# Optimization experiments

Measured on AMD Instinct MI355X. Metric: run time of the kernel, lower is better.

The kernel has to match this reference:

```python
import jax, jax.numpy as jnp
import numpy as np

C = 256      # in_channels
NH = 4       # n_heads
NG = 32      # GroupNorm num_groups
EPS = 1e-5   # torch GroupNorm default eps


def _conv1x1(x, w, b):
    # 1x1 conv == per-pixel channel matmul. x: (B,C,H,W), w: (O,C), b: (O,)
    return jnp.einsum('oc,bchw->bohw', w, x) + b[None, :, None, None]


def _groupnorm(x, gamma, beta):
    b, c, h, w = x.shape
    xg = x.reshape(b, NG, c // NG, h, w)
    mu = xg.mean(axis=(2, 3, 4), keepdims=True)
    var = xg.var(axis=(2, 3, 4), keepdims=True)
    xn = ((xg - mu) * jax.lax.rsqrt(var + EPS)).reshape(b, c, h, w)
    return xn * gamma[None, :, None, None] + beta[None, :, None, None]


def setup_inputs() -> dict:
    key = jax.random.key(0)
    ks = jax.random.split(key, 5)
    B, H, W = 2, 64, 64
    s = 1.0 / np.sqrt(C).astype(np.float32)
    return {
        'x': jax.random.normal(ks[0], (B, C, H, W), jnp.float32),
        'gamma': jnp.ones((C,), jnp.float32),
        'beta': jnp.zeros((C,), jnp.float32),
        'wq': jax.random.normal(ks[1], (C, C), jnp.float32) * s,
        'bq': jnp.zeros((C,), jnp.float32),
        'wk': jax.random.normal(ks[2], (C, C), jnp.float32) * s,
        'bk': jnp.zeros((C,), jnp.float32),
        'wv': jax.random.normal(ks[3], (C, C), jnp.float32) * s,
        'bv': jnp.zeros((C,), jnp.float32),
        'wp': jax.random.normal(ks[4], (C, C), jnp.float32) * s,
        'bp': jnp.zeros((C,), jnp.float32),
    }


def reference(x, gamma, beta, wq, bq, wk, bk, wv, bv, wp, bp):
    b, c, h, w = x.shape
    c_ = c // NH  # head dim
    hn = _groupnorm(x, gamma, beta)
    # NOTE: original splits channels as (head_dim, n_heads) with head_dim leading
    q = _conv1x1(hn, wq, bq).reshape(b, c_, NH, h * w)
    k = _conv1x1(hn, wk, bk).reshape(b, c_, NH, h * w)
    v = _conv1x1(hn, wv, bv).reshape(b, c_, NH, h * w)
    scores = jnp.einsum('bcnq,bcnk->bqkn', q, k) * (c_ ** -0.5)  # (B,S,S,NH)
    attn = jax.nn.softmax(scores, axis=2)  # softmax over key axis
    out = jnp.einsum('bcnd,bqdn->bcnq', v, attn).reshape(b, c, h, w)
    return x + _conv1x1(out, wp, bp)
```

## Files before the change

kernel.cpp:

```cpp
#include <hip/hip_runtime.h>

#define CH 256
#define NHEAD 4
#define HD 64
#define SP 4096
#define NB 2
#define QSCALE 0.1803368801111204f

typedef __attribute__((ext_vector_type(8))) short bf16x8;
typedef __attribute__((ext_vector_type(4))) float f32x4;
typedef unsigned int u32;
typedef unsigned short u16;

__device__ inline u16 b16(float f) {
    u32 u = __float_as_uint(f);
    return (u16)((u + 0x8000u) >> 16);
}
__device__ inline float fexp2(float x) { return __builtin_amdgcn_exp2f(x); }

__global__ __launch_bounds__(256) void prep_kernel(
    const float* __restrict__ x, float2* __restrict__ part,
    const float* __restrict__ wq, const float* __restrict__ wk,
    const float* __restrict__ wv, const float* __restrict__ wp,
    u16* __restrict__ wqb, u16* __restrict__ wkb,
    u16* __restrict__ wvb, u16* __restrict__ wpb)
{
    int tid = threadIdx.x;
    if (blockIdx.x < 256) {
        int bgq = blockIdx.x;
        int bg = bgq >> 2, qtr = bgq & 3;
        const float4* xp = (const float4*)(x + (size_t)bg * 8 * SP) + qtr * 2048;
        float s = 0.f, ss = 0.f;
        for (int i = tid; i < 2048; i += 256) {
            float4 u = xp[i];
            s  += (u.x + u.y) + (u.z + u.w);
            ss += (u.x * u.x + u.y * u.y) + (u.z * u.z + u.w * u.w);
        }
#pragma unroll
        for (int off = 32; off > 0; off >>= 1) {
            s  += __shfl_down(s, off);
            ss += __shfl_down(ss, off);
        }
        __shared__ float ws_s[4], ws_q[4];
        int w = tid >> 6;
        if ((tid & 63) == 0) { ws_s[w] = s; ws_q[w] = ss; }
        __syncthreads();
        if (tid == 0)
            part[bgq] = make_float2(ws_s[0] + ws_s[1] + ws_s[2] + ws_s[3],
                                    ws_q[0] + ws_q[1] + ws_q[2] + ws_q[3]);
    } else {
        int idx = (blockIdx.x - 256) * 256 + tid;
        int m = idx >> 16, i = idx & 65535;
        if (m == 0)      wqb[i] = b16(wq[i] * QSCALE);
        else if (m == 1) wkb[i] = b16(wk[i]);
        else if (m == 2) wvb[i] = b16(wv[i]);
        else {
            int c = i >> 8, chan = i & 255;
            int n = chan >> 6, d = chan & 63;
            wpb[i] = b16(wp[c * 256 + d * 4 + n]);
        }
    }
}

__global__ __launch_bounds__(256) void qkv_gemm_kernel(
    const float* __restrict__ x, const float2* __restrict__ part,
    const float* __restrict__ gamma, const float* __restrict__ beta,
    const u16* __restrict__ wqb, const u16* __restrict__ wkb,
    const u16* __restrict__ wvb,
    const float* __restrict__ bq, const float* __restrict__ bk,
    const float* __restrict__ bv,
    u16* __restrict__ qt, u16* __restrict__ ktp, u16* __restrict__ vtp)
{
    int zz = blockIdx.y;
    int b = zz / 3, p = zz % 3;
    const u16* W = (p == 0) ? wqb : (p == 1) ? wkb : wvb;
    const float* bias = (p == 0) ? bq : (p == 1) ? bk : bv;
    float bs = (p == 0) ? QSCALE : 1.f;
    int s0 = blockIdx.x * 16;
    int tid = threadIdx.x, w = tid >> 6, lane = tid & 63;
    int t = lane >> 4, ln = lane & 15;

    __shared__ u16 SB[6144];
    __shared__ float As[256], Bs[256];

    {
        int c = tid, bg = b * 32 + (c >> 3);
        float s = 0.f, ss = 0.f;
#pragma unroll
        for (int q = 0; q < 4; q++) { float2 pp = part[bg * 4 + q]; s += pp.x; ss += pp.y; }
        float mu = s * (1.f / 32768.f);
        float var = ss * (1.f / 32768.f) - mu * mu;
        float rs = rsqrtf(var + 1e-5f);
        float ga = gamma[c];
        As[c] = rs * ga;
        Bs[c] = beta[c] - mu * rs * ga;
    }
    __syncthreads();

    {
        int cb = tid >> 2, sseg = (tid & 3) * 4;
#pragma unroll
        for (int it = 0; it < 4; it++) {
            int c = it * 64 + cb;
            float4 v = *(const float4*)&x[((size_t)b * CH + c) * SP + s0 + sseg];
            float aa = As[c], bb = Bs[c];
            SB[(sseg + 0) * 264 + c] = b16(fmaf(aa, v.x, bb));
            SB[(sseg + 1) * 264 + c] = b16(fmaf(aa, v.y, bb));
            SB[(sseg + 2) * 264 + c] = b16(fmaf(aa, v.z, bb));
            SB[(sseg + 3) * 264 + c] = b16(fmaf(aa, v.w, bb));
        }
    }
    __syncthreads();

    f32x4 acc[4];
#pragma unroll
    for (int og = 0; og < 4; og++)
        acc[og] = (f32x4){0.f, 0.f, 0.f, 0.f};

#pragma unroll
    for (int ks = 0; ks < 8; ks++) {
        bf16x8 af[4];
#pragma unroll
        for (int og = 0; og < 4; og++)
            af[og] = *(const bf16x8*)&W[(size_t)(w * 64 + og * 16 + ln) * CH + ks * 32 + t * 8];
        bf16x8 bfv = *(const bf16x8*)&SB[ln * 264 + ks * 32 + t * 8];
#pragma unroll
        for (int og = 0; og < 4; og++)
            acc[og] = __builtin_amdgcn_mfma_f32_16x16x32_bf16(
                af[og], bfv, acc[og], 0, 0, 0);
    }
    __syncthreads();

    if (p < 2) {
#pragma unroll
        for (int og = 0; og < 4; og++)
#pragma unroll
            for (int r = 0; r < 4; r++) {
                int o = w * 64 + og * 16 + 4 * t + r;
                SB[(r * 16 + ln) * 72 + (w * 16 + og * 4 + t)] =
                    b16(acc[og][r] + bias[o] * bs);
            }
        __syncthreads();
        if (p == 0) {
#pragma unroll
            for (int it = 0; it < 2; it++) {
                int f = it * 256 + tid;
                int o8 = f & 7, sl = (f >> 3) & 15, n = f >> 7;
                *(uint4*)&qt[((size_t)(b * 4 + n) * SP + s0 + sl) * HD + o8 * 8] =
                    *(const uint4*)&SB[(n * 16 + sl) * 72 + o8 * 8];
            }
        } else {
#pragma unroll
            for (int it = 0; it < 2; it++) {
                int f = it * 256 + tid;
                int o8 = f & 7, sl = (f >> 3) & 15, n = f >> 7;
                int key = s0 + sl;
                int g = ((key >> 4) & 3) * 2 + (o8 >> 2);
                int lp = (key & 15) + 16 * (o8 & 3);
                *(uint4*)&ktp[(size_t)(b * 4 + n) * SP * HD +
                              (size_t)(key >> 6) * 4096 + g * 512 + lp * 8] =
                    *(const uint4*)&SB[(n * 16 + sl) * 72 + o8 * 8];
            }
        }
    } else {
#pragma unroll
        for (int og = 0; og < 4; og++)
#pragma unroll
            for (int r = 0; r < 4; r++) {
                int o = w * 64 + og * 16 + 4 * t + r;
                SB[(r * 64 + w * 16 + og * 4 + t) * 24 + ln] =
                    b16(acc[og][r] + bias[o]);
            }
        __syncthreads();
#pragma unroll
        for (int it = 0; it < 2; it++) {
            int f = it * 256 + tid;
            int so8 = f & 1, d = (f >> 1) & 63, n = f >> 7;
            int key = s0 + so8 * 8;
            int g = ((d >> 4) & 3) * 2 + ((key >> 5) & 1);
            int lp = (d & 15) + 16 * ((key >> 3) & 3);
            *(uint4*)&vtp[(size_t)(b * 4 + n) * SP * HD +
                          (size_t)(key >> 6) * 4096 + g * 512 + lp * 8] =
                *(const uint4*)&SB[(n * 64 + d) * 24 + so8 * 8];
        }
    }
}

template <int NT>
__global__ __launch_bounds__(256, 3) void attn_kernel(
    const u16* __restrict__ qtb, const u16* __restrict__ ktp,
    const u16* __restrict__ vtp, u16* __restrict__ opart,
    float* __restrict__ lpart)
{
    int bx = blockIdx.x;
    int z = bx & 7, qt_i = (bx >> 3) & 31, sp = bx >> 8;
    int sq0 = qt_i * 128;
    int tile0 = sp * NT;
    const u16* qz = qtb + (size_t)z * SP * HD;
    const u16* kz = ktp + (size_t)z * SP * HD;
    const u16* vz = vtp + (size_t)z * SP * HD;

    int tid = threadIdx.x, w = tid >> 6, l = tid & 63;
    int t = l >> 4, ln = l & 15;

    __shared__ __align__(16) u32 Pb[4][2][512];

    bf16x8 qf[2][2];
#pragma unroll
    for (int qg = 0; qg < 2; qg++)
#pragma unroll
        for (int ds = 0; ds < 2; ds++)
            qf[qg][ds] = *(const bf16x8*)&qz[
                (size_t)(sq0 + w * 32 + qg * 16 + ln) * HD + ds * 32 + t * 8];

    bf16x8 kf[8], vf[8];
#pragma unroll
    for (int g = 0; g < 8; g++)
        kf[g] = *(const bf16x8*)&kz[(size_t)tile0 * 4096 + g * 512 + l * 8];

    float lsum[2] = {0.f, 0.f};
    f32x4 oacc[2][4];
#pragma unroll
    for (int qg = 0; qg < 2; qg++)
#pragma unroll
        for (int dg = 0; dg < 4; dg++)
            oacc[qg][dg] = (f32x4){0.f, 0.f, 0.f, 0.f};

    const f32x4 z4 = {0.f, 0.f, 0.f, 0.f};
    f32x4 sa[2][4];

    auto ep = [&](int qg) {
#pragma unroll
        for (int kg = 0; kg < 4; kg++) {
            float e0 = fexp2(sa[qg][kg][0]);
            float e1 = fexp2(sa[qg][kg][1]);
            float e2 = fexp2(sa[qg][kg][2]);
            float e3 = fexp2(sa[qg][kg][3]);
            lsum[qg] += (e0 + e1) + (e2 + e3);
            u32 p0 = __builtin_amdgcn_perm(__float_as_uint(e1), __float_as_uint(e0), 0x07060302u);
            u32 p1 = __builtin_amdgcn_perm(__float_as_uint(e3), __float_as_uint(e2), 0x07060302u);
            int Lt = ln + 16 * (2 * (kg & 1) + (t >> 1));
            int ksg = kg >> 1;
            *(uint2*)&Pb[w][qg][(ksg * 64 + Lt) * 4 + 2 * (t & 1)] =
                make_uint2(p0, p1);
        }
    };

#pragma unroll
    for (int kti = 0; kti < NT; kti++) {
        size_t tb = (size_t)(tile0 + kti) * 4096;

#pragma unroll
        for (int g = 0; g < 8; g++)
            vf[g] = *(const bf16x8*)&vz[tb + g * 512 + l * 8];

#pragma unroll
        for (int kg = 0; kg < 4; kg++)
#pragma unroll
            for (int qg = 0; qg < 2; qg++)
                sa[qg][kg] = __builtin_amdgcn_mfma_f32_16x16x32_bf16(
                    kf[kg * 2 + 0], qf[qg][0], z4, 0, 0, 0);
#pragma unroll
        for (int kg = 0; kg < 4; kg++)
#pragma unroll
            for (int qg = 0; qg < 2; qg++)
                sa[qg][kg] = __builtin_amdgcn_mfma_f32_16x16x32_bf16(
                    kf[kg * 2 + 1], qf[qg][1], sa[qg][kg], 0, 0, 0);

        if (kti < NT - 1) {
            size_t nb = tb + 4096;
#pragma unroll
            for (int g = 0; g < 8; g++)
                kf[g] = *(const bf16x8*)&kz[nb + g * 512 + l * 8];
        }

        ep(0);
#pragma unroll
        for (int qg = 0; qg < 2; qg++) {
            if (qg == 0) ep(1);
            bf16x8 pf[2];
#pragma unroll
            for (int ksg = 0; ksg < 2; ksg++)
                pf[ksg] = *(const bf16x8*)&Pb[w][qg][(ksg * 64 + l) * 4];
#pragma unroll
            for (int ksg = 0; ksg < 2; ksg++)
#pragma unroll
                for (int dg = 0; dg < 4; dg++)
                    oacc[qg][dg] = __builtin_amdgcn_mfma_f32_16x16x32_bf16(
                        pf[ksg], vf[dg * 2 + ksg], oacc[qg][dg], 0, 0, 0);
        }
    }

#pragma unroll
    for (int qg = 0; qg < 2; qg++) {
        lsum[qg] += __shfl_xor(lsum[qg], 16);
        lsum[qg] += __shfl_xor(lsum[qg], 32);
    }

    size_t obase = (size_t)(sp * 8 + z) * SP;
    u16* po = (u16*)&Pb[w][0][0];
#pragma unroll
    for (int qg = 0; qg < 2; qg++)
#pragma unroll
        for (int dg = 0; dg < 4; dg++)
#pragma unroll
            for (int r = 0; r < 4; r++)
                po[(qg * 16 + 4 * t + r) * 64 + dg * 16 + ln] = b16(oacc[qg][dg][r]);
#pragma unroll
    for (int i = 0; i < 4; i++) {
        int f = i * 512 + l * 8;
        int qloc = f >> 6, d0 = f & 63;
        uint4 v = *(const uint4*)&po[f];
        *(uint4*)&opart[(obase + sq0 + w * 32 + qloc) * HD + d0] = v;
    }
    if (t == 0)
#pragma unroll
        for (int qg = 0; qg < 2; qg++)
            lpart[obase + sq0 + w * 32 + qg * 16 + ln] = lsum[qg];
}

template <int NSPLIT>
__global__ __launch_bounds__(256) void proj_gemm_kernel(
    const u16* __restrict__ opart, const float* __restrict__ lpart,
    const u16* __restrict__ wpb, const float* __restrict__ bp,
    const float* __restrict__ x, float* __restrict__ out)
{
    int b = blockIdx.y;
    int s0 = blockIdx.x * 16;
    int tid = threadIdx.x, w = tid >> 6, lane = tid & 63;
    int t = lane >> 4, ln = lane & 15;

    __shared__ u16 BsL[16 * 264];

#pragma unroll
    for (int it = 0; it < 2; it++) {
        int f = it * 256 + tid;
        int oct = f & 31, s = f >> 5;
        int n = oct >> 3, d0 = (oct & 7) * 8;
        float lsumv = 0.f;
        float accv[8] = {0.f,0.f,0.f,0.f,0.f,0.f,0.f,0.f};
#pragma unroll
        for (int sp = 0; sp < NSPLIT; sp++) {
            size_t base = (size_t)(sp * 8 + b * 4 + n) * SP + s0 + s;
            lsumv += lpart[base];
            uint4 o4 = *(const uint4*)&opart[base * HD + d0];
            u32 ov[4] = {o4.x, o4.y, o4.z, o4.w};
#pragma unroll
            for (int i = 0; i < 4; i++) {
                accv[2 * i + 0] += __uint_as_float(ov[i] << 16);
                accv[2 * i + 1] += __uint_as_float(ov[i] & 0xffff0000u);
            }
        }
        float inv = 1.f / lsumv;
        u32 res[4];
#pragma unroll
        for (int i = 0; i < 4; i++) {
            u16 rl = b16(accv[2 * i + 0] * inv);
            u16 rh = b16(accv[2 * i + 1] * inv);
            res[i] = ((u32)rh << 16) | rl;
        }
        *(uint4*)&BsL[s * 264 + oct * 8] = make_uint4(res[0], res[1], res[2], res[3]);
    }
    __syncthreads();

    f32x4 acc[4];
#pragma unroll
    for (int og = 0; og < 4; og++)
        acc[og] = (f32x4){0.f, 0.f, 0.f, 0.f};

#pragma unroll
    for (int ks = 0; ks < 8; ks++) {
        bf16x8 af[4];
#pragma unroll
        for (int og = 0; og < 4; og++)
            af[og] = *(const bf16x8*)&wpb[(size_t)(w * 64 + og * 16 + ln) * CH + ks * 32 + t * 8];
        bf16x8 bfv = *(const bf16x8*)&BsL[ln * 264 + ks * 32 + t * 8];
#pragma unroll
        for (int og = 0; og < 4; og++)
            acc[og] = __builtin_amdgcn_mfma_f32_16x16x32_bf16(
                af[og], bfv, acc[og], 0, 0, 0);
    }

#pragma unroll
    for (int og = 0; og < 4; og++)
#pragma unroll
        for (int r = 0; r < 4; r++) {
            int c = w * 64 + og * 16 + 4 * t + r;
            size_t idx = ((size_t)b * CH + c) * SP + s0 + ln;
            out[idx] = acc[og][r] + bp[c] + x[idx];
        }
}

extern "C" void kernel_launch(void* const* d_in, const int* in_sizes, int n_in,
                              void* d_out, int out_size, void* d_ws, size_t ws_size,
                              hipStream_t stream)
{
    const float* x     = (const float*)d_in[0];
    const float* gamma = (const float*)d_in[1];
    const float* beta  = (const float*)d_in[2];
    const float* wq = (const float*)d_in[3]; const float* bq = (const float*)d_in[4];
    const float* wk = (const float*)d_in[5]; const float* bk = (const float*)d_in[6];
    const float* wv = (const float*)d_in[7]; const float* bv = (const float*)d_in[8];
    const float* wp = (const float*)d_in[9]; const float* bp = (const float*)d_in[10];
    float* out = (float*)d_out;

    const size_t TEN = (size_t)8 * SP * HD;
    const size_t NEED8 = 4096 + 524288 + 3 * TEN * 2 + 8 * TEN * 2 + 8 * 8 * SP * 4;
    int nsplit = (ws_size >= NEED8) ? 8 : 4;

    char* wsb = (char*)d_ws;
    float2* part = (float2*)wsb;
    u16* wqb = (u16*)(wsb + 4096);
    u16* wkb = wqb + 65536;
    u16* wvb = wkb + 65536;
    u16* wpb = wvb + 65536;
    u16* qt  = wpb + 65536;
    u16* ktp = qt + TEN;
    u16* vtp = ktp + TEN;
    u16* opart = vtp + TEN;
    float* lpart = (float*)(opart + (size_t)nsplit * TEN);

    prep_kernel<<<dim3(1280), dim3(256), 0, stream>>>(
        x, part, wq, wk, wv, wp, wqb, wkb, wvb, wpb);
    qkv_gemm_kernel<<<dim3(256, 6), dim3(256), 0, stream>>>(
        x, part, gamma, beta, wqb, wkb, wvb, bq, bk, bv, qt, ktp, vtp);
    if (nsplit == 8) {
        attn_kernel<8><<<dim3(2048), dim3(256), 0, stream>>>(
            qt, ktp, vtp, opart, lpart);
        proj_gemm_kernel<8><<<dim3(256, 2), dim3(256), 0, stream>>>(
            opart, lpart, wpb, bp, x, out);
    } else {
        attn_kernel<16><<<dim3(1024), dim3(256), 0, stream>>>(
            qt, ktp, vtp, opart, lpart);
        proj_gemm_kernel<4><<<dim3(256, 2), dim3(256), 0, stream>>>(
            opart, lpart, wpb, bp, x, out);
    }
}
```

Before: 165.8 us.

## Enlarge QKV GEMM and attention tiles, use 512-thread attention blocks

The QKV GEMM now handles 32 spatial positions per block with two accumulator groups, so each weight fragment is reused across two B fragments. The attention kernel moves to 512-thread blocks covering 256 queries and always uses the 4-way key split, so K/V loads are shared by more waves. A block-wide barrier is added at the top of each key tile, and the wp bf16 conversion now writes in scattered order instead of reading scattered. The trade-offs are fewer blocks in flight, higher register and LDS pressure, and extra synchronisation in the attention loop.

```diff
diff --git a/kernel.cpp b/kernel.cpp
--- a/kernel.cpp
+++ b/kernel.cpp
@@ -55,9 +55,9 @@
         else if (m == 1) wkb[i] = b16(wk[i]);
         else if (m == 2) wvb[i] = b16(wv[i]);
         else {
-            int c = i >> 8, chan = i & 255;
-            int n = chan >> 6, d = chan & 63;
-            wpb[i] = b16(wp[c * 256 + d * 4 + n]);
+            int c = i >> 8, col = i & 255;
+            int n = col & 3, d = col >> 2;
+            wpb[c * 256 + n * 64 + d] = b16(wp[i]);
         }
     }
 }
@@ -76,11 +76,11 @@
     const u16* W = (p == 0) ? wqb : (p == 1) ? wkb : wvb;
     const float* bias = (p == 0) ? bq : (p == 1) ? bk : bv;
     float bs = (p == 0) ? QSCALE : 1.f;
-    int s0 = blockIdx.x * 16;
+    int s0 = blockIdx.x * 32;
     int tid = threadIdx.x, w = tid >> 6, lane = tid & 63;
     int t = lane >> 4, ln = lane & 15;
 
-    __shared__ u16 SB[6144];
+    __shared__ u16 SB[10240];
     __shared__ float As[256], Bs[256];
 
     {
@@ -98,10 +98,10 @@
     __syncthreads();
 
     {
-        int cb = tid >> 2, sseg = (tid & 3) * 4;
-#pragma unroll
-        for (int it = 0; it < 4; it++) {
-            int c = it * 64 + cb;
+        int cb = tid >> 3, sseg = (tid & 7) * 4;
+#pragma unroll
+        for (int it = 0; it < 8; it++) {
+            int c = it * 32 + cb;
             float4 v = *(const float4*)&x[((size_t)b * CH + c) * SP + s0 + sseg];
             float aa = As[c], bb = Bs[c];
             SB[(sseg + 0) * 264 + c] = b16(fmaf(aa, v.x, bb));
@@ -112,22 +112,28 @@
     }
     __syncthreads();
 
-    f32x4 acc[4];
+    f32x4 acc[4][2];
 #pragma unroll
     for (int og = 0; og < 4; og++)
-        acc[og] = (f32x4){0.f, 0.f, 0.f, 0.f};
+#pragma unroll
+        for (int sg = 0; sg < 2; sg++)
+            acc[og][sg] = (f32x4){0.f, 0.f, 0.f, 0.f};
 
 #pragma unroll
     for (int ks = 0; ks < 8; ks++) {
-        bf16x8 af[4];
+        bf16x8 af[4], bfv[2];
 #pragma unroll
         for (int og = 0; og < 4; og++)
             af[og] = *(const bf16x8*)&W[(size_t)(w * 64 + og * 16 + ln) * CH + ks * 32 + t * 8];
-        bf16x8 bfv = *(const bf16x8*)&SB[ln * 264 + ks * 32 + t * 8];
-#pragma unroll
-        for (int og = 0; og < 4; og++)
-            acc[og] = __builtin_amdgcn_mfma_f32_16x16x32_bf16(
-                af[og], bfv, acc[og], 0, 0, 0);
+#pragma unroll
+        for (int sg = 0; sg < 2; sg++)
+            bfv[sg] = *(const bf16x8*)&SB[(sg * 16 + ln) * 264 + ks * 32 + t * 8];
+#pragma unroll
+        for (int og = 0; og < 4; og++)
+#pragma unroll
+            for (int sg = 0; sg < 2; sg++)
+                acc[og][sg] = __builtin_amdgcn_mfma_f32_16x16x32_bf16(
+                    af[og], bfv[sg], acc[og][sg], 0, 0, 0);
     }
     __syncthreads();
 
@@ -135,66 +141,70 @@
 #pragma unroll
         for (int og = 0; og < 4; og++)
 #pragma unroll
-            for (int r = 0; r < 4; r++) {
-                int o = w * 64 + og * 16 + 4 * t + r;
-                SB[(r * 16 + ln) * 72 + (w * 16 + og * 4 + t)] =
-                    b16(acc[og][r] + bias[o] * bs);
-            }
+            for (int sg = 0; sg < 2; sg++)
+#pragma unroll
+                for (int r = 0; r < 4; r++) {
+                    int o = w * 64 + og * 16 + 4 * t + r;
+                    SB[(r * 32 + sg * 16 + ln) * 72 + (w * 16 + og * 4 + t)] =
+                        b16(acc[og][sg][r] + bias[o] * bs);
+                }
         __syncthreads();
         if (p == 0) {
 #pragma unroll
-            for (int it = 0; it < 2; it++) {
+            for (int it = 0; it < 4; it++) {
                 int f = it * 256 + tid;
-                int o8 = f & 7, sl = (f >> 3) & 15, n = f >> 7;
+                int o8 = f & 7, sl = (f >> 3) & 31, n = f >> 8;
                 *(uint4*)&qt[((size_t)(b * 4 + n) * SP + s0 + sl) * HD + o8 * 8] =
-                    *(const uint4*)&SB[(n * 16 + sl) * 72 + o8 * 8];
+                    *(const uint4*)&SB[(n * 32 + sl) * 72 + o8 * 8];
             }
         } else {
 #pragma unroll
-            for (int it = 0; it < 2; it++) {
+            for (int it = 0; it < 4; it++) {
                 int f = it * 256 + tid;
-                int o8 = f & 7, sl = (f >> 3) & 15, n = f >> 7;
+                int o8 = f & 7, sl = (f >> 3) & 31, n = f >> 8;
                 int key = s0 + sl;
                 int g = ((key >> 4) & 3) * 2 + (o8 >> 2);
                 int lp = (key & 15) + 16 * (o8 & 3);
                 *(uint4*)&ktp[(size_t)(b * 4 + n) * SP * HD +
                               (size_t)(key >> 6) * 4096 + g * 512 + lp * 8] =
-                    *(const uint4*)&SB[(n * 16 + sl) * 72 + o8 * 8];
+                    *(const uint4*)&SB[(n * 32 + sl) * 72 + o8 * 8];
             }
         }
     } else {
 #pragma unroll
         for (int og = 0; og < 4; og++)
 #pragma unroll
-            for (int r = 0; r < 4; r++) {
-                int o = w * 64 + og * 16 + 4 * t + r;
-                SB[(r * 64 + w * 16 + og * 4 + t) * 24 + ln] =
-                    b16(acc[og][r] + bias[o]);
-            }
+            for (int sg = 0; sg < 2; sg++)
+#pragma unroll
+                for (int r = 0; r < 4; r++) {
+                    int o = w * 64 + og * 16 + 4 * t + r;
+                    SB[(r * 64 + w * 16 + og * 4 + t) * 40 + sg * 16 + ln] =
+                        b16(acc[og][sg][r] + bias[o]);
+                }
         __syncthreads();
 #pragma unroll
-        for (int it = 0; it < 2; it++) {
+        for (int it = 0; it < 4; it++) {
             int f = it * 256 + tid;
-            int so8 = f & 1, d = (f >> 1) & 63, n = f >> 7;
+            int so8 = f & 3, d = (f >> 2) & 63, n = f >> 8;
             int key = s0 + so8 * 8;
             int g = ((d >> 4) & 3) * 2 + ((key >> 5) & 1);
             int lp = (d & 15) + 16 * ((key >> 3) & 3);
             *(uint4*)&vtp[(size_t)(b * 4 + n) * SP * HD +
                           (size_t)(key >> 6) * 4096 + g * 512 + lp * 8] =
-                *(const uint4*)&SB[(n * 64 + d) * 24 + so8 * 8];
+                *(const uint4*)&SB[(n * 64 + d) * 40 + so8 * 8];
         }
     }
 }
 
 template <int NT>
-__global__ __launch_bounds__(256, 3) void attn_kernel(
+__global__ __launch_bounds__(512) void attn_kernel(
     const u16* __restrict__ qtb, const u16* __restrict__ ktp,
     const u16* __restrict__ vtp, u16* __restrict__ opart,
     float* __restrict__ lpart)
 {
     int bx = blockIdx.x;
-    int z = bx & 7, qt_i = (bx >> 3) & 31, sp = bx >> 8;
-    int sq0 = qt_i * 128;
+    int z = bx & 7, qt_i = (bx >> 3) & 15, sp = bx >> 7;
+    int sq0 = qt_i * 256;
     int tile0 = sp * NT;
     const u16* qz = qtb + (size_t)z * SP * HD;
     const u16* kz = ktp + (size_t)z * SP * HD;
@@ -203,7 +213,7 @@
     int tid = threadIdx.x, w = tid >> 6, l = tid & 63;
     int t = l >> 4, ln = l & 15;
 
-    __shared__ __align__(16) u32 Pb[4][2][512];
+    __shared__ __align__(16) u32 Pb[8][2][512];
 
     bf16x8 qf[2][2];
 #pragma unroll
@@ -250,6 +260,8 @@
     for (int kti = 0; kti < NT; kti++) {
         size_t tb = (size_t)(tile0 + kti) * 4096;
 
+        __syncthreads();
+
 #pragma unroll
         for (int g = 0; g < 8; g++)
             vf[g] = *(const bf16x8*)&vz[tb + g * 512 + l * 8];
@@ -405,9 +417,6 @@
     float* out = (float*)d_out;
 
     const size_t TEN = (size_t)8 * SP * HD;
-    const size_t NEED8 = 4096 + 524288 + 3 * TEN * 2 + 8 * TEN * 2 + 8 * 8 * SP * 4;
-    int nsplit = (ws_size >= NEED8) ? 8 : 4;
-
     char* wsb = (char*)d_ws;
     float2* part = (float2*)wsb;
     u16* wqb = (u16*)(wsb + 4096);
@@ -418,21 +427,14 @@
     u16* ktp = qt + TEN;
     u16* vtp = ktp + TEN;
     u16* opart = vtp + TEN;
-    float* lpart = (float*)(opart + (size_t)nsplit * TEN);
+    float* lpart = (float*)(opart + (size_t)4 * TEN);
 
     prep_kernel<<<dim3(1280), dim3(256), 0, stream>>>(
         x, part, wq, wk, wv, wp, wqb, wkb, wvb, wpb);
-    qkv_gemm_kernel<<<dim3(256, 6), dim3(256), 0, stream>>>(
+    qkv_gemm_kernel<<<dim3(128, 6), dim3(256), 0, stream>>>(
         x, part, gamma, beta, wqb, wkb, wvb, bq, bk, bv, qt, ktp, vtp);
-    if (nsplit == 8) {
-        attn_kernel<8><<<dim3(2048), dim3(256), 0, stream>>>(
-            qt, ktp, vtp, opart, lpart);
-        proj_gemm_kernel<8><<<dim3(256, 2), dim3(256), 0, stream>>>(
-            opart, lpart, wpb, bp, x, out);
-    } else {
-        attn_kernel<16><<<dim3(1024), dim3(256), 0, stream>>>(
-            qt, ktp, vtp, opart, lpart);
-        proj_gemm_kernel<4><<<dim3(256, 2), dim3(256), 0, stream>>>(
-            opart, lpart, wpb, bp, x, out);
-    }
-}
+    attn_kernel<16><<<dim3(512), dim3(512), 0, stream>>>(
+        qt, ktp, vtp, opart, lpart);
+    proj_gemm_kernel<4><<<dim3(256, 2), dim3(256), 0, stream>>>(
+        opart, lpart, wpb, bp, x, out);
+}
```

Result: no change. 163.7 us (-1.3%).
